# Kernel tuning notes

Measured on AMD Instinct MI355X. Metric: run time of the kernel, lower is better.

Reference implementation:

```python
import jax, jax.numpy as jnp
import numpy as np

NUM_REC = 22
P = 24            # nodes per graph
G = 8192          # graphs in batch
N = G * P         # 196608 nodes
E = N * 4         # 786432 edges (avg degree 4)
F_NODE = 96       # 74 chem features + 22 receptor one-hot
F_EDGE = 16
EPS = 1e-5
NEG_SLOPE = 0.2   # GATv2 default negative_slope


def gatv2(x, src, dst, edge_attr, Wl, bl, Wr, br, We, att, bo):
    """PyG GATv2Conv (heads=1, add_self_loops=True, fill_value='mean'), eval mode."""
    n = x.shape[0]
    # self loops with edge_attr = mean of incoming edge attrs per target node
    deg = jax.ops.segment_sum(jnp.ones_like(dst, dtype=x.dtype), dst, num_segments=n)
    loop_attr = jax.ops.segment_sum(edge_attr, dst, num_segments=n) / jnp.maximum(deg, 1.0)[:, None]
    loop = jnp.arange(n, dtype=src.dtype)
    s = jnp.concatenate([src, loop])           # [E+N] source
    d = jnp.concatenate([dst, loop])           # [E+N] target
    ea = jnp.concatenate([edge_attr, loop_attr], axis=0)
    xl = x @ Wl + bl                           # source transform [n, C]
    xr = x @ Wr + br                           # target transform [n, C]
    m = xl[s] + xr[d] + ea @ We                # [E+N, C]
    e = jax.nn.leaky_relu(m, NEG_SLOPE) @ att  # [E+N] attention logits
    # segment softmax over target nodes (every node has its self loop -> no empty segment)
    emax = jax.ops.segment_max(e, d, num_segments=n)
    ez = jnp.exp(e - emax[d])
    denom = jax.ops.segment_sum(ez, d, num_segments=n)
    alpha = ez / denom[d]
    return jax.ops.segment_sum(alpha[:, None] * xl[s], d, num_segments=n) + bo


def batchnorm(h, gamma, beta):
    # training-style BN (batch statistics, biased var) as in torch BatchNorm1d forward
    mu = h.mean(0)
    var = h.var(0)
    return gamma * (h - mu) * jax.lax.rsqrt(var + EPS) + beta


def setup_inputs() -> dict:
    key = jax.random.key(0)
    ks = jax.random.split(key, 40)
    x = jax.random.normal(ks[0], (N, F_NODE), jnp.float32)
    # intra-graph, self-loop-free edges
    src = jax.random.randint(ks[1], (E,), 0, N)
    off = jax.random.randint(ks[2], (E,), 1, P)
    dst = (src // P) * P + (src % P + off) % P
    edge_index = jnp.stack([src, dst]).astype(jnp.int32)
    edge_attr = jax.random.normal(ks[3], (E, F_EDGE), jnp.float32)
    batch = (jnp.arange(N) // P).astype(jnp.int32)

    def lin(k, i, o):
        return jax.random.normal(k, (i, o), jnp.float32) * 0.1

    def vec(k, o):
        return jax.random.normal(k, (o,), jnp.float32) * 0.1

    Fin = F_NODE - NUM_REC  # 74
    return {
        "x": x, "edge_index": edge_index, "edge_attr": edge_attr, "batch": batch,
        # GATv2 layer 1 (74 -> 32)
        "Wl1": lin(ks[4], Fin, 32), "bl1": vec(ks[5], 32),
        "Wr1": lin(ks[6], Fin, 32), "br1": vec(ks[7], 32),
        "We1": lin(ks[8], F_EDGE, 32), "att1": vec(ks[9], 32), "bo1": vec(ks[10], 32),
        # GATv2 layer 2 (32 -> 8)
        "Wl2": lin(ks[11], 32, 8), "bl2": vec(ks[12], 8),
        "Wr2": lin(ks[13], 32, 8), "br2": vec(ks[14], 8),
        "We2": lin(ks[15], F_EDGE, 8), "att2": vec(ks[16], 8), "bo2": vec(ks[17], 8),
        # BatchNorm affine
        "g1": jnp.ones((32,), jnp.float32), "be1": jnp.zeros((32,), jnp.float32),
        "g2": jnp.ones((8,), jnp.float32), "be2": jnp.zeros((8,), jnp.float32),
        # MLP head (8+22=30 -> 32 -> 16 -> 8 -> 4 -> 2)
        "fc1_W": lin(ks[18], 8 + NUM_REC, 32), "fc1_b": vec(ks[19], 32),
        "fc2_W": lin(ks[20], 32, 16), "fc2_b": vec(ks[21], 16),
        "fc3_W": lin(ks[22], 16, 8), "fc3_b": vec(ks[23], 8),
        "fc4_W": lin(ks[24], 8, 4), "fc4_b": vec(ks[25], 4),
        "out_W": lin(ks[26], 4, 2), "out_b": vec(ks[27], 2),
    }


def reference(x, edge_index, edge_attr, batch,
              Wl1, bl1, Wr1, br1, We1, att1, bo1,
              Wl2, bl2, Wr2, br2, We2, att2, bo2,
              g1, be1, g2, be2,
              fc1_W, fc1_b, fc2_W, fc2_b, fc3_W, fc3_b, fc4_W, fc4_b, out_W, out_b):
    src, dst = edge_index[0], edge_index[1]
    # per-graph receptor features = last NUM_REC cols of the first node of each graph
    first_idx = jnp.searchsorted(batch, jnp.arange(G, dtype=batch.dtype))
    rec_feat = x[first_idx, -NUM_REC:]                       # [G, 22]
    xin = x[:, :-NUM_REC]                                    # [N, 74]

    h = jax.nn.relu(gatv2(xin, src, dst, edge_attr, Wl1, bl1, Wr1, br1, We1, att1, bo1))
    h = batchnorm(h, g1, be1)                                # [N, 32]
    h = jax.nn.sigmoid(gatv2(h, src, dst, edge_attr, Wl2, bl2, Wr2, br2, We2, att2, bo2))
    h = batchnorm(h, g2, be2)                                # [N, 8]

    cnt = jax.ops.segment_sum(jnp.ones((x.shape[0], 1), x.dtype), batch, num_segments=G)
    pooled = jax.ops.segment_sum(h, batch, num_segments=G) / cnt  # global_mean_pool [G, 8]

    z = jnp.concatenate([pooled, rec_feat], axis=1)          # [G, 30]
    z = jax.nn.relu(z @ fc1_W + fc1_b)
    z = jax.nn.relu(z @ fc2_W + fc2_b)
    z = jax.nn.relu(z @ fc3_W + fc3_b)
    z = jax.nn.relu(z @ fc4_W + fc4_b)
    return z @ out_W + out_b                                 # [G, 2]
```

## Files before the change

### kernel.cpp

```cpp
#include <hip/hip_runtime.h>

typedef unsigned short u16;
typedef unsigned int   u32;
typedef __attribute__((ext_vector_type(4))) float f4_t;
typedef __attribute__((ext_vector_type(4))) unsigned short us4_t;

#define GG 8192
#define PP 24
#define NN 196608
#define EE 786432
#define CAP 176

#define oWl1 0
#define oWr1 2368
#define obl1 4736
#define obr1 4768
#define oWe1 4800
#define oatt1 5312
#define obo1 5344
#define oWl2 5376
#define oWr2 5632
#define obl2 5888
#define obr2 5896
#define oWe2 5904
#define oatt2 6032
#define obo2 6040
#define ofc1W 6048
#define ofc1b 7008
#define ofc2W 7040
#define ofc2b 7552
#define ofc3W 7568
#define ofc3b 7696
#define ofc4W 7704
#define ofc4b 7736
#define ooutW 7740
#define ooutb 7748

#define oW1I 0
#define oW2P 4864
#define oB2P 5376

__device__ __forceinline__ float bf2f(u16 u){
  union { u32 i; float f; } x; x.i = ((u32)u) << 16; return x.f;
}
__device__ __forceinline__ u32 fkey(float f){
  int i = __float_as_int(f);
  return (i >= 0) ? (((u32)i) | 0x80000000u) : ~((u32)i);
}
__device__ __forceinline__ float funkey(u32 k){
  u32 i = (k & 0x80000000u) ? (k & 0x7FFFFFFFu) : ~k;
  return __uint_as_float(i);
}
__device__ __forceinline__ float lrelu(float m){ return m > 0.f ? m : 0.2f*m; }
__device__ __forceinline__ float sexp(float a){ return __expf(fminf(a, 0.f)); }
__device__ __forceinline__ float ldf(const void* p, size_t i, int isf){
  return isf ? ((const float*)p)[i] : bf2f(((const u16*)p)[i]);
}

__global__ void k_zero(float* __restrict__ out){
  int i = blockIdx.x*256 + threadIdx.x;
  if(i < GG*2) out[i] = 0.f;
}

__global__ void k_count(const int* __restrict__ dst, int* __restrict__ cnt){
  int e = blockIdx.x*256 + threadIdx.x;
  if(e < EE){
    u32 d = (u32)dst[e];
    if(d < (u32)NN) atomicAdd(&cnt[d], 1);
  }
}

__global__ void k_scanA(const int* __restrict__ cnt, int* __restrict__ offs,
                        int* __restrict__ bsum){
  __shared__ int part[1024];
  int t = threadIdx.x;
  int i = blockIdx.x*1024 + t;
  int c = cnt[i];
  part[t] = c; __syncthreads();
  for(int off=1; off<1024; off<<=1){
    int v = (t>=off) ? part[t-off] : 0;
    __syncthreads();
    part[t] += v;
    __syncthreads();
  }
  offs[i] = part[t] - c;
  if(t==1023) bsum[blockIdx.x] = part[1023];
}

__global__ void k_scanB(int* __restrict__ bsum, int* __restrict__ offs){
  __shared__ int part[256];
  int t = threadIdx.x;
  int c = (t < 192) ? bsum[t] : 0;
  part[t] = c; __syncthreads();
  for(int off=1; off<256; off<<=1){
    int v = (t>=off) ? part[t-off] : 0;
    __syncthreads();
    part[t] += v;
    __syncthreads();
  }
  if(t < 192) bsum[t] = part[t] - c;
  if(t == 255) offs[NN] = part[255];
}

__global__ void k_scanC(int* __restrict__ offs, const int* __restrict__ bsum,
                        int* __restrict__ cursor){
  int t = threadIdx.x;
  int i = blockIdx.x*1024 + t;
  int v = offs[i] + bsum[blockIdx.x];
  offs[i] = v;
  cursor[i] = v;
}

__global__ void k_scatter(const int* __restrict__ src, const int* __restrict__ dst,
                          int* __restrict__ cursor, int* __restrict__ spack){
  int e = blockIdx.x*256 + threadIdx.x;
  if(e < EE){
    u32 d = (u32)dst[e];
    if(d >= (u32)NN) return;
    int g = d / PP;
    int pos = atomicAdd(&cursor[d], 1);
    if((u32)pos < (u32)EE){
      int sl = src[e] - g*PP;
      if((u32)sl > 23u) sl = 0;
      spack[pos] = sl | ((int)(d - g*PP) << 5) | (e << 10);
    }
  }
}

__global__ void k_eaperm(const int* __restrict__ spack, const int* __restrict__ offs,
                         const void* __restrict__ ea, const int* __restrict__ dflag,
                         float* __restrict__ eap){
  int i = blockIdx.x*256 + threadIdx.x;
  if(i >= EE) return;
  if(i >= offs[NN]) return;
  int isf = dflag[0];
  u32 id = ((u32)spack[i]) >> 10;
  if(id >= (u32)EE) id = 0;
  float* o = eap + (size_t)i*16;
  if(isf){
    const float* er = (const float*)ea + (size_t)id*16;
    #pragma unroll
    for(int q=0;q<4;q++) *(f4_t*)(o + q*4) = *(const f4_t*)(er + q*4);
  } else {
    const u16* er = (const u16*)ea + (size_t)id*16;
    #pragma unroll
    for(int c=0;c<16;c++) o[c] = bf2f(er[c]);
  }
}

__global__ void k_eapermP(const int* __restrict__ spack, const int* __restrict__ offs,
                          const void* __restrict__ ea, const int* __restrict__ dflag,
                          const float* __restrict__ wb,
                          float* __restrict__ p1, float* __restrict__ p2){
  int i = blockIdx.x*256 + threadIdx.x;
  if(i >= EE) return;
  if(i >= offs[NN]) return;
  int isf = dflag[0];
  u32 id = ((u32)spack[i]) >> 10;
  if(id >= (u32)EE) id = 0;
  float eav[16];
  if(isf){
    const float* er = (const float*)ea + (size_t)id*16;
    #pragma unroll
    for(int k=0;k<16;k++) eav[k] = er[k];
  } else {
    const u16* er = (const u16*)ea + (size_t)id*16;
    #pragma unroll
    for(int k=0;k<16;k++) eav[k] = bf2f(er[k]);
  }
  float* o1 = p1 + (size_t)i*32;
  #pragma unroll
  for(int c=0;c<32;c+=4){
    float s0=0.f, s1=0.f, s2=0.f, s3=0.f;
    #pragma unroll
    for(int k=0;k<16;k++){
      f4_t w = *(const f4_t*)(wb + oWe1 + k*32 + c);
      s0 += eav[k]*w[0]; s1 += eav[k]*w[1]; s2 += eav[k]*w[2]; s3 += eav[k]*w[3];
    }
    f4_t r; r[0]=s0; r[1]=s1; r[2]=s2; r[3]=s3;
    *(f4_t*)(o1 + c) = r;
  }
  float* o2 = p2 + (size_t)i*8;
  #pragma unroll
  for(int c=0;c<8;c+=4){
    float s0=0.f, s1=0.f, s2=0.f, s3=0.f;
    #pragma unroll
    for(int k=0;k<16;k++){
      f4_t w = *(const f4_t*)(wb + oWe2 + k*8 + c);
      s0 += eav[k]*w[0]; s1 += eav[k]*w[1]; s2 += eav[k]*w[2]; s3 += eav[k]*w[3];
    }
    f4_t r; r[0]=s0; r[1]=s1; r[2]=s2; r[3]=s3;
    *(f4_t*)(o2 + c) = r;
  }
}

__global__ void k_wconv(float* __restrict__ wb, float* __restrict__ wq, int* __restrict__ dflag,
    const u32* __restrict__ xw,
    const void* Wl1, const void* bl1, const void* Wr1, const void* br1,
    const void* We1, const void* att1, const void* bo1,
    const void* Wl2, const void* bl2, const void* Wr2, const void* br2,
    const void* We2, const void* att2, const void* bo2,
    const void* f1W, const void* f1b, const void* f2W, const void* f2b,
    const void* f3W, const void* f3b, const void* f4W, const void* f4b,
    const void* oW,  const void* ob)
{
  __shared__ u32 mx[256];
  int t = threadIdx.x;
  u32 m = 0;
  for(int i=t; i<2048; i+=256){
    u32 e = (xw[i] >> 7) & 0xFFu;
    m = m > e ? m : e;
  }
  mx[t] = m; __syncthreads();
  for(int off=128; off>0; off>>=1){
    if(t<off) mx[t] = mx[t] > mx[t+off] ? mx[t] : mx[t+off];
    __syncthreads();
  }
  int isf = (mx[0] > 140u) ? 1 : 0;
  if(t==0) dflag[0] = isf;
  #define CP(off,src,len) for(int i=t;i<(len);i+=256) wb[(off)+i]=ldf(src,i,isf);
  CP(oWl1,Wl1,2368) CP(oWr1,Wr1,2368) CP(obl1,bl1,32) CP(obr1,br1,32)
  CP(oWe1,We1,512)  CP(oatt1,att1,32) CP(obo1,bo1,32)
  CP(oWl2,Wl2,256)  CP(oWr2,Wr2,256)  CP(obl2,bl2,8)  CP(obr2,br2,8)
  CP(oWe2,We2,128)  CP(oatt2,att2,8)  CP(obo2,bo2,8)
  CP(ofc1W,f1W,960) CP(ofc1b,f1b,32)  CP(ofc2W,f2W,512) CP(ofc2b,f2b,16)
  CP(ofc3W,f3W,128) CP(ofc3b,f3b,8)   CP(ofc4W,f4W,32)  CP(ofc4b,f4b,4)
  CP(ooutW,oW,8)    CP(ooutb,ob,2)
  #undef CP
  for(int i=t; i<76*64; i+=256){
    int k = i>>6, cc = i&63, mat = cc>>5, c = cc&31;
    wq[oW1I + i] = (k < 74) ? ldf(mat ? Wr1 : Wl1, k*32 + c, isf) : 0.f;
  }
}

__global__ void k_prep2(float* __restrict__ wq, const float* __restrict__ wb,
                        const float* __restrict__ stats1){
  int t = threadIdx.x;
  for(int i=t; i<512; i+=256){
    int k = i>>4, cc = i&15, mat = cc>>3, c = cc&7;
    wq[oW2P + i] = stats1[k] * wb[(mat ? oWr2 : oWl2) + k*8 + c];
  }
  if(t < 16){
    int mat = t>>3, c = t&7;
    float s = wb[(mat ? obr2 : obl2) + c];
    for(int k=0;k<32;k++) s += stats1[32+k] * wb[(mat ? oWr2 : oWl2) + k*8 + c];
    wq[oB2P + t] = s;
  }
}

__global__ __launch_bounds__(256, 6) void k_l1stats_p(
    const void* __restrict__ x, const float* __restrict__ p1,
    const float* __restrict__ wb, const float* __restrict__ wq,
    const int* __restrict__ offs, const int* __restrict__ spack, const int* __restrict__ dflag,
    float* __restrict__ p1sum, float* __restrict__ p1sq,
    float* __restrict__ h1)
{
  __shared__ __align__(16) float sXl[24][36];
  __shared__ __align__(16) float sXr[24][36];
  __shared__ __align__(16) float sPS[24][32];
  __shared__ __align__(16) float sPQ[24][32];
  __shared__ float sEv[CAP];
  __shared__ int   sSl[CAP];
  __shared__ int   sRO[25];

  const int t = threadIdx.x;
  const int g = blockIdx.x;
  const int isf = dflag[0];
  const int nb = g*PP;
  const int eb = offs[nb];
  int ecnt = offs[nb+24] - eb;
  if(ecnt < 0) ecnt = 0; if(ecnt > CAP) ecnt = CAP;

  if(t < 25){
    int v = offs[nb+t] - eb;
    if(v < 0) v = 0; if(v > CAP) v = CAP;
    sRO[t] = v;
  }
  for(int i=t; i<ecnt; i+=256){
    int sl = spack[eb+i] & 31; if(sl > 23) sl = 0;
    sSl[i] = sl;
  }

  {
    const int c = t & 31, mat = (t>>5)&1, w = t>>6, cc = t&63;
    const float* gW = wq + oW1I;
    float bi = wb[(mat ? obr1 : obl1) + c];
    float acc[6];
    #pragma unroll
    for(int j=0;j<6;j++) acc[j] = bi;
    if(isf){
      const float* xr0 = (const float*)x + (size_t)(nb + w*6)*96;
      for(int kb=0; kb<19; kb++){
        float w0 = gW[(kb*4+0)*64 + cc];
        float w1 = gW[(kb*4+1)*64 + cc];
        float w2 = gW[(kb*4+2)*64 + cc];
        float w3 = gW[(kb*4+3)*64 + cc];
        #pragma unroll
        for(int j=0;j<6;j++){
          f4_t xv = *(const f4_t*)(xr0 + (size_t)j*96 + kb*4);
          acc[j] += xv[0]*w0 + xv[1]*w1 + xv[2]*w2 + xv[3]*w3;
        }
      }
    } else {
      const u16* xr0 = (const u16*)x + (size_t)(nb + w*6)*96;
      for(int kb=0; kb<19; kb++){
        float w0 = gW[(kb*4+0)*64 + cc];
        float w1 = gW[(kb*4+1)*64 + cc];
        float w2 = gW[(kb*4+2)*64 + cc];
        float w3 = gW[(kb*4+3)*64 + cc];
        #pragma unroll
        for(int j=0;j<6;j++){
          us4_t xv = *(const us4_t*)(xr0 + (size_t)j*96 + kb*4);
          acc[j] += bf2f(xv[0])*w0 + bf2f(xv[1])*w1 + bf2f(xv[2])*w2 + bf2f(xv[3])*w3;
        }
      }
    }
    if(mat){
      #pragma unroll
      for(int j=0;j<6;j++) sXr[w*6+j][c] = acc[j];
    } else {
      #pragma unroll
      for(int j=0;j<6;j++) sXl[w*6+j][c] = acc[j];
    }
  }
  __syncthreads();

  if(t < 192){
    const int r = t >> 3, sub = t & 7;
    const int a = sRO[r], b = sRO[r+1];
    const int deg = b - a;
    const float* att = wb + oatt1;

    float emax = -3.4e38f;
    for(int e=a+sub; e<b; e+=8){
      int sl = sSl[e];
      const float* pe = p1 + (size_t)(eb+e)*32;
      float ev = 0.f;
      #pragma unroll
      for(int q=0;q<8;q++){
        f4_t pv  = *(const f4_t*)(pe + q*4);
        f4_t xlv = *(const f4_t*)&sXl[sl][q*4];
        f4_t xrv = *(const f4_t*)&sXr[r][q*4];
        ev += att[q*4+0]*lrelu(xlv[0]+xrv[0]+pv[0]);
        ev += att[q*4+1]*lrelu(xlv[1]+xrv[1]+pv[1]);
        ev += att[q*4+2]*lrelu(xlv[2]+xrv[2]+pv[2]);
        ev += att[q*4+3]*lrelu(xlv[3]+xrv[3]+pv[3]);
      }
      sEv[e] = ev;
      emax = fmaxf(emax, ev);
    }
    emax = fmaxf(emax, __shfl_xor(emax, 1));
    emax = fmaxf(emax, __shfl_xor(emax, 2));
    emax = fmaxf(emax, __shfl_xor(emax, 4));

    float m0=0.f, m1=0.f, m2=0.f, m3=0.f;
    for(int e=a; e<b; ++e){
      f4_t pv = *(const f4_t*)(p1 + (size_t)(eb+e)*32 + sub*4);
      m0 += pv[0]; m1 += pv[1]; m2 += pv[2]; m3 += pv[3];
    }
    float invd = 1.f / (float)(deg > 0 ? deg : 1);
    float sv;
    {
      int c0 = sub*4;
      sv  = att[c0+0]*lrelu(sXl[r][c0+0] + sXr[r][c0+0] + m0*invd);
      sv += att[c0+1]*lrelu(sXl[r][c0+1] + sXr[r][c0+1] + m1*invd);
      sv += att[c0+2]*lrelu(sXl[r][c0+2] + sXr[r][c0+2] + m2*invd);
      sv += att[c0+3]*lrelu(sXl[r][c0+3] + sXr[r][c0+3] + m3*invd);
    }
    sv += __shfl_xor(sv, 1);
    sv += __shfl_xor(sv, 2);
    sv += __shfl_xor(sv, 4);

    float m = fmaxf(emax, sv);
    float ssum = 0.f;
    for(int e=a+sub; e<b; e+=8){
      float z = sexp(sEv[e] - m);
      sEv[e] = z;
      ssum += z;
    }
    ssum += __shfl_xor(ssum, 1);
    ssum += __shfl_xor(ssum, 2);
    ssum += __shfl_xor(ssum, 4);
    float selfZ = sexp(sv - m);
    float rden = 1.f / fmaxf(ssum + selfZ, 1e-30f);

    float a0=0.f, a1=0.f, a2=0.f, a3=0.f;
    for(int e=a; e<b; ++e){
      float z = sEv[e];
      f4_t xlv = *(const f4_t*)&sXl[sSl[e]][sub*4];
      a0 += z*xlv[0]; a1 += z*xlv[1]; a2 += z*xlv[2]; a3 += z*xlv[3];
    }
    f4_t xself = *(const f4_t*)&sXl[r][sub*4];
    f4_t outv, sqv;
    {
      float o;
      o = (a0 + selfZ*xself[0]) * rden; o = fmaxf(o + wb[obo1+sub*4+0], 0.f); outv[0]=o; sqv[0]=o*o;
      o = (a1 + selfZ*xself[1]) * rden; o = fmaxf(o + wb[obo1+sub*4+1], 0.f); outv[1]=o; sqv[1]=o*o;
      o = (a2 + selfZ*xself[2]) * rden; o = fmaxf(o + wb[obo1+sub*4+2], 0.f); outv[2]=o; sqv[2]=o*o;
      o = (a3 + selfZ*xself[3]) * rden; o = fmaxf(o + wb[obo1+sub*4+3], 0.f); outv[3]=o; sqv[3]=o*o;
    }
    *(f4_t*)&h1[((size_t)nb + r)*32 + sub*4] = outv;
    *(f4_t*)&sPS[r][sub*4] = outv;
    *(f4_t*)&sPQ[r][sub*4] = sqv;
  }
  __syncthreads();
  if(t < 32){
    float s=0.f, q=0.f;
    #pragma unroll
    for(int r=0;r<24;r++){ s += sPS[r][t]; q += sPQ[r][t]; }
    p1sum[g*32+t] = s; p1sq[g*32+t] = q;
  }
}

__global__ __launch_bounds__(256, 6) void k_fused2_p(
    const float* __restrict__ p2,
    const float* __restrict__ wb, const float* __restrict__ wq,
    const float* __restrict__ h1,
    const int* __restrict__ offs, const int* __restrict__ spack,
    float* __restrict__ gsum2, float* __restrict__ gsq2)
{
  __shared__ float sXl2[24][13];
  __shared__ float sXr2[24][13];
  __shared__ float sEv[CAP];
  __shared__ int   sSl[CAP];
  __shared__ int   sRO[25];
  __shared__ float sGS[24][8];
  __shared__ float sGQ[24][8];

  const int t = threadIdx.x;
  const int g = blockIdx.x;
  const int wid = t >> 6;
  const int lane = t & 63;
  const int nb = g*PP;
  const int eb = offs[nb];
  int ecnt = offs[nb+24] - eb;
  if(ecnt < 0) ecnt = 0; if(ecnt > CAP) ecnt = CAP;

  if(t < 25){
    int v = offs[nb+t] - eb;
    if(v < 0) v = 0; if(v > CAP) v = CAP;
    sRO[t] = v;
  }
  for(int i=t; i<ecnt; i+=256){
    int sl = spack[eb+i] & 31; if(sl > 23) sl = 0;
    sSl[i] = sl;
  }
  {
    int rz = wid*6;
    for(int i=lane; i<96; i+=64){
      int rl = i>>4, cc = i&15;
      int r = rz + rl;
      float s = wq[oB2P + cc];
      const float* hr = h1 + ((size_t)nb + r)*32;
      #pragma unroll
      for(int q=0;q<8;q++){
        f4_t hv = *(const f4_t*)(hr + q*4);
        s += hv[0]*wq[oW2P+(q*4+0)*16+cc] + hv[1]*wq[oW2P+(q*4+1)*16+cc]
           + hv[2]*wq[oW2P+(q*4+2)*16+cc] + hv[3]*wq[oW2P+(q*4+3)*16+cc];
      }
      if(cc < 8) sXl2[r][cc] = s; else sXr2[r][cc-8] = s;
    }
  }
  __syncthreads();

  if(t < 192){
    const int r = t >> 3, sub = t & 7;
    const int a = sRO[r], b = sRO[r+1];
    const int deg = b - a;
    const float* att2 = wb + oatt2;

    float emax = -3.4e38f;
    for(int e=a+sub; e<b; e+=8){
      int sl = sSl[e];
      const float* pe = p2 + (size_t)(eb+e)*8;
      float ev = 0.f;
      #pragma unroll
      for(int j=0;j<8;j++)
        ev += att2[j]*lrelu(sXl2[sl][j] + sXr2[r][j] + pe[j]);
      sEv[e] = ev;
      emax = fmaxf(emax, ev);
    }
    emax = fmaxf(emax, __shfl_xor(emax, 1));
    emax = fmaxf(emax, __shfl_xor(emax, 2));
    emax = fmaxf(emax, __shfl_xor(emax, 4));

    float mpc = 0.f;
    for(int e=a; e<b; ++e)
      mpc += p2[(size_t)(eb+e)*8 + sub];
    float invd = 1.f / (float)(deg > 0 ? deg : 1);
    float sv = att2[sub]*lrelu(sXl2[r][sub] + sXr2[r][sub] + mpc*invd);
    sv += __shfl_xor(sv, 1);
    sv += __shfl_xor(sv, 2);
    sv += __shfl_xor(sv, 4);

    float m = fmaxf(emax, sv);
    float ssum = 0.f;
    for(int e=a+sub; e<b; e+=8){
      float z = sexp(sEv[e] - m);
      sEv[e] = z;
      ssum += z;
    }
    ssum += __shfl_xor(ssum, 1);
    ssum += __shfl_xor(ssum, 2);
    ssum += __shfl_xor(ssum, 4);
    float selfZ = sexp(sv - m);
    float rden = 1.f / fmaxf(ssum + selfZ, 1e-30f);

    float acc = 0.f;
    for(int e=a; e<b; ++e)
      acc += sEv[e] * sXl2[sSl[e]][sub];
    float o = (acc + selfZ*sXl2[r][sub]) * rden;
    float s = 1.f / (1.f + __expf(-(o + wb[obo2+sub])));
    sGS[r][sub] = s;
    sGQ[r][sub] = s*s;
  }
  __syncthreads();
  if(t < 8){
    float gs=0.f, gq=0.f;
    #pragma unroll
    for(int r=0;r<24;r++){ gs += sGS[r][t]; gq += sGQ[r][t]; }
    gsum2[g*8+t] = gs; gsq2[g*8+t] = gq;
  }
}

__global__ __launch_bounds__(256, 6) void k_l1stats(
    const void* __restrict__ x, const void* __restrict__ ea, const float* __restrict__ eap,
    const float* __restrict__ wb, const float* __restrict__ wq,
    const int* __restrict__ offs, const int* __restrict__ spack, const int* __restrict__ dflag,
    float* __restrict__ p1sum, float* __restrict__ p1sq,
    float* __restrict__ h1, int use_h1)
{
  __shared__ __align__(16) float sEaF[CAP][16];
  __shared__ __align__(16) float sXl[24][36];
  __shared__ float sXr[24][33];
  __shared__ float sEaSum[24][17];
  __shared__ float sEv[CAP];
  __shared__ int   sSl[CAP];
  __shared__ int   sRO[25];
  __shared__ float sSelfE[24];
  __shared__ float sPS[4][32], sPQ[4][32];

  const int t = threadIdx.x;
  const int g = blockIdx.x;
  const int wid = t >> 6;
  const int lane = t & 63;
  const int isf = dflag[0];
  const int nb = g*PP;
  const int eb = offs[nb];
  int ecnt = offs[nb+24] - eb; if(ecnt < 0) ecnt = 0; if(ecnt > CAP) ecnt = CAP;

  if(t < 25){
    int v = offs[nb+t] - eb;
    if(v < 0) v = 0; if(v > CAP) v = CAP;
    sRO[t] = v;
  }
  if(eap){
    for(int i=t; i<ecnt; i+=256) sSl[i] = spack[eb+i] & 1023;
    for(int i=t; i<ecnt*4; i+=256){
      int e = i>>2, q = i&3;
      *(f4_t*)&sEaF[e][q*4] = *(const f4_t*)(eap + ((size_t)(eb+e))*16 + q*4);
    }
  } else {
    for(int i=t; i<ecnt; i+=256){
      int sp = spack[eb+i];
      sSl[i] = sp & 1023;
      u32 id = ((u32)sp) >> 10;
      if(id >= (u32)EE) id = 0;
      if(isf){
        const float* er = (const float*)ea + (size_t)id*16;
        #pragma unroll
        for(int q=0;q<4;q++) *(f4_t*)&sEaF[i][q*4] = *(const f4_t*)(er + q*4);
      } else {
        #pragma unroll
        for(int c=0;c<16;c++) sEaF[i][c] = bf2f(((const u16*)ea)[(size_t)id*16 + c]);
      }
    }
  }
  {
    int rz = wid*6;
    for(int i=lane; i<6*17; i+=64) sEaSum[rz + i/17][i%17] = 0.f;
  }

  {
    const int c = t & 31, mat = (t>>5)&1, w = wid, cc = t&63;
    const float* gW = wq + oW1I;
    float bi = wb[(mat ? obr1 : obl1) + c];
    float acc[6];
    #pragma unroll
    for(int j=0;j<6;j++) acc[j] = bi;
    if(isf){
      const float* xr0 = (const float*)x + (size_t)(nb + w*6)*96;
      for(int kb=0; kb<19; kb++){
        float w0 = gW[(kb*4+0)*64 + cc];
        float w1 = gW[(kb*4+1)*64 + cc];
        float w2 = gW[(kb*4+2)*64 + cc];
        float w3 = gW[(kb*4+3)*64 + cc];
        #pragma unroll
        for(int j=0;j<6;j++){
          f4_t xv = *(const f4_t*)(xr0 + (size_t)j*96 + kb*4);
          acc[j] += xv[0]*w0 + xv[1]*w1 + xv[2]*w2 + xv[3]*w3;
        }
      }
    } else {
      const u16* xr0 = (const u16*)x + (size_t)(nb + w*6)*96;
      for(int kb=0; kb<19; kb++){
        float w0 = gW[(kb*4+0)*64 + cc];
        float w1 = gW[(kb*4+1)*64 + cc];
        float w2 = gW[(kb*4+2)*64 + cc];
        float w3 = gW[(kb*4+3)*64 + cc];
        #pragma unroll
        for(int j=0;j<6;j++){
          us4_t xv = *(const us4_t*)(xr0 + (size_t)j*96 + kb*4);
          acc[j] += bf2f(xv[0])*w0 + bf2f(xv[1])*w1 + bf2f(xv[2])*w2 + bf2f(xv[3])*w3;
        }
      }
    }
    if(mat){
      #pragma unroll
      for(int j=0;j<6;j++) sXr[w*6+j][c] = acc[j];
    } else {
      #pragma unroll
      for(int j=0;j<6;j++) sXl[w*6+j][c] = acc[j];
    }
  }
  __syncthreads();

  const int r0 = wid*6;
  const int a0 = sRO[r0], a1 = sRO[r0+6];
  const int c = t & 31, eo = (t>>5)&1;

  float wr[16];
  #pragma unroll
  for(int k=0;k<16;k++) wr[k] = wb[oWe1 + k*32 + c];
  const float av = wb[oatt1 + c];
  const float bv = wb[obo1 + c];

  for(int base=a0; base<a1; base+=2){
    int e = base + eo;
    bool valid = (e < a1);
    int ec = valid ? e : a0;
    int sp = sSl[ec];
    int sl = sp & 31; if(sl > 23) sl = 0;
    int dl = (sp >> 5) & 31; if(dl > 23) dl = 0;
    f4_t A0 = *(const f4_t*)&sEaF[ec][0];
    f4_t A1 = *(const f4_t*)&sEaF[ec][4];
    f4_t A2 = *(const f4_t*)&sEaF[ec][8];
    f4_t A3 = *(const f4_t*)&sEaF[ec][12];
    float p = A0[0]*wr[0]+A0[1]*wr[1]+A0[2]*wr[2]+A0[3]*wr[3]
            + A1[0]*wr[4]+A1[1]*wr[5]+A1[2]*wr[6]+A1[3]*wr[7]
            + A2[0]*wr[8]+A2[1]*wr[9]+A2[2]*wr[10]+A2[3]*wr[11]
            + A3[0]*wr[12]+A3[1]*wr[13]+A3[2]*wr[14]+A3[3]*wr[15];
    if(valid && c < 16) atomicAdd(&sEaSum[dl][c], sEaF[ec][c]);
    float v = lrelu(sXl[sl][c] + sXr[dl][c] + p) * av;
    v += __shfl_xor(v, 16);
    v += __shfl_xor(v, 8);
    v += __shfl_xor(v, 4);
    v += __shfl_xor(v, 2);
    v += __shfl_xor(v, 1);
    if(valid && c == 0) sEv[e] = v;
  }

  #pragma unroll
  for(int rp=0; rp<3; rp++){
    int r = r0 + rp*2 + eo;
    int deg = sRO[r+1] - sRO[r];
    float invd = 1.f / (float)(deg > 0 ? deg : 1);
    float mp = 0.f;
    #pragma unroll
    for(int k=0;k<16;k++) mp += sEaSum[r][k] * wr[k];
    float v = lrelu(sXl[r][c] + sXr[r][c] + mp*invd) * av;
    v += __shfl_xor(v, 16);
    v += __shfl_xor(v, 8);
    v += __shfl_xor(v, 4);
    v += __shfl_xor(v, 2);
    v += __shfl_xor(v, 1);
    if(c == 0) sSelfE[r] = v;
  }

  float ps = 0.f, pq = 0.f;
  const int h = (t >> 5) & 1;
  #pragma unroll
  for(int j=0;j<6;j++){
    int r = r0 + j;
    int a = sRO[r], b = sRO[r+1];
    float selfE = sSelfE[r];
    float mx = -3.4e38f;
    for(int e=a+lane; e<b; e+=64) mx = fmaxf(mx, sEv[e]);
    mx = fmaxf(mx, __shfl_xor(mx, 32));
    mx = fmaxf(mx, __shfl_xor(mx, 16));
    mx = fmaxf(mx, __shfl_xor(mx, 8));
    mx = fmaxf(mx, __shfl_xor(mx, 4));
    mx = fmaxf(mx, __shfl_xor(mx, 2));
    mx = fmaxf(mx, __shfl_xor(mx, 1));
    float m = fmaxf(mx, selfE);
    float ds = 0.f;
    for(int e=a+lane; e<b; e+=64){
      float z = sexp(sEv[e] - m);
      sEv[e] = z;
      ds += z;
    }
    ds += __shfl_xor(ds, 32);
    ds += __shfl_xor(ds, 16);
    ds += __shfl_xor(ds, 8);
    ds += __shfl_xor(ds, 4);
    ds += __shfl_xor(ds, 2);
    ds += __shfl_xor(ds, 1);
    float selfZ = sexp(selfE - m);
    float rden = 1.f / fmaxf(ds + selfZ, 1e-30f);
    float acc = 0.f;
    for(int e=a+h; e<b; e+=2){
      int sl = sSl[e] & 31; if(sl > 23) sl = 0;
      acc += sEv[e] * sXl[sl][c];
    }
    acc += __shfl_xor(acc, 32);
    float out = (acc + selfZ * sXl[r][c]) * rden;
    out = fmaxf(out + bv, 0.f);
    if(h == 0){
      if(use_h1) h1[((size_t)nb + r)*32 + c] = out;
      ps += out; pq += out*out;
    }
  }
  if(h == 0){ sPS[wid][c] = ps; sPQ[wid][c] = pq; }
  __syncthreads();
  if(t < 32){
    p1sum[g*32+t] = sPS[0][t]+sPS[1][t]+sPS[2][t]+sPS[3][t];
    p1sq[g*32+t]  = sPQ[0][t]+sPQ[1][t]+sPQ[2][t]+sPQ[3][t];
  }
}

__global__ void k_reduce(const float* __restrict__ ps, const float* __restrict__ pq,
                         const void* __restrict__ gamma, const void* __restrict__ beta,
                         const int* __restrict__ dflag,
                         float* __restrict__ stats, int F){
  __shared__ float rs[256], rq[256];
  int f = blockIdx.x, t = threadIdx.x;
  float s=0.f, q=0.f;
  for(int g=t; g<GG; g+=256){ s += ps[g*F+f]; q += pq[g*F+f]; }
  rs[t]=s; rq[t]=q; __syncthreads();
  for(int off=128; off>0; off>>=1){
    if(t<off){ rs[t]+=rs[t+off]; rq[t]+=rq[t+off]; }
    __syncthreads();
  }
  if(t==0){
    int isf = dflag[0];
    float mu  = rs[0] * (1.f/(float)NN);
    float var = rq[0] * (1.f/(float)NN) - mu*mu;
    if(var < 0.f) var = 0.f;
    float sc  = ldf(gamma,f,isf) / sqrtf(var + 1e-5f);
    stats[f]   = sc;
    stats[F+f] = ldf(beta,f,isf) - mu*sc;
  }
}

__global__ __launch_bounds__(256, 6) void k_fused2_h1(
    const void* __restrict__ ea, const float* __restrict__ eap,
    const float* __restrict__ wb, const float* __restrict__ wq,
    const float* __restrict__ h1,
    const int* __restrict__ offs, const int* __restrict__ spack, const int* __restrict__ dflag,
    float* __restrict__ gsum2, float* __restrict__ gsq2)
{
  __shared__ __align__(16) float sEaF[CAP][16];
  __shared__ float sXl2[24][12], sXr2[24][12];
  __shared__ float sEaSum[24][17];
  __shared__ float sEv[CAP];
  __shared__ int   sSl[CAP];
  __shared__ int   sRO[25];
  __shared__ float sSelfE[24];
  __shared__ float sGS[4][8], sGQ[4][8];

  const int t = threadIdx.x;
  const int g = blockIdx.x;
  const int wid = t >> 6;
  const int lane = t & 63;
  const int isf = dflag[0];
  const int nb = g*PP;
  const int eb = offs[nb];
  int ecnt = offs[nb+24] - eb; if(ecnt < 0) ecnt = 0; if(ecnt > CAP) ecnt = CAP;

  if(t < 25){
    int v = offs[nb+t] - eb;
    if(v < 0) v = 0; if(v > CAP) v = CAP;
    sRO[t] = v;
  }
  if(eap){
    for(int i=t; i<ecnt; i+=256) sSl[i] = spack[eb+i] & 1023;
    for(int i=t; i<ecnt*4; i+=256){
      int e = i>>2, q = i&3;
      *(f4_t*)&sEaF[e][q*4] = *(const f4_t*)(eap + ((size_t)(eb+e))*16 + q*4);
    }
  } else {
    for(int i=t; i<ecnt; i+=256){
      int sp = spack[eb+i];
      sSl[i] = sp & 1023;
      u32 id = ((u32)sp) >> 10;
      if(id >= (u32)EE) id = 0;
      if(isf){
        const float* er = (const float*)ea + (size_t)id*16;
        #pragma unroll
        for(int q=0;q<4;q++) *(f4_t*)&sEaF[i][q*4] = *(const f4_t*)(er + q*4);
      } else {
        #pragma unroll
        for(int c=0;c<16;c++) sEaF[i][c] = bf2f(((const u16*)ea)[(size_t)id*16 + c]);
      }
    }
  }
  {
    int rz = wid*6;
    for(int i=lane; i<6*17; i+=64) sEaSum[rz + i/17][i%17] = 0.f;
    for(int i=lane; i<96; i+=64){
      int rl = i>>4, cc = i&15;
      int r = rz + rl;
      float s = wq[oB2P + cc];
      const float* hr = h1 + ((size_t)nb + r)*32;
      #pragma unroll
      for(int q=0;q<8;q++){
        f4_t hv = *(const f4_t*)(hr + q*4);
        s += hv[0]*wq[oW2P+(q*4+0)*16+cc] + hv[1]*wq[oW2P+(q*4+1)*16+cc]
           + hv[2]*wq[oW2P+(q*4+2)*16+cc] + hv[3]*wq[oW2P+(q*4+3)*16+cc];
      }
      if(cc < 8) sXl2[r][cc] = s; else sXr2[r][cc-8] = s;
    }
  }
  __syncthreads();

  const int r0 = wid*6;
  const int a0 = sRO[r0], a1 = sRO[r0+6];
  const int c = t & 7;
  const int eo = lane >> 3;

  float wr[16];
  #pragma unroll
  for(int k=0;k<16;k++) wr[k] = wb[oWe2 + k*8 + c];
  const float av = wb[oatt2 + c];
  const float bv = wb[obo2 + c];

  for(int base=a0; base<a1; base+=8){
    int e = base + eo;
    bool valid = (e < a1);
    int ec = valid ? e : a0;
    int sp = sSl[ec];
    int sl = sp & 31; if(sl > 23) sl = 0;
    int dl = (sp >> 5) & 31; if(dl > 23) dl = 0;
    f4_t A0 = *(const f4_t*)&sEaF[ec][0];
    f4_t A1 = *(const f4_t*)&sEaF[ec][4];
    f4_t A2 = *(const f4_t*)&sEaF[ec][8];
    f4_t A3 = *(const f4_t*)&sEaF[ec][12];
    float p = A0[0]*wr[0]+A0[1]*wr[1]+A0[2]*wr[2]+A0[3]*wr[3]
            + A1[0]*wr[4]+A1[1]*wr[5]+A1[2]*wr[6]+A1[3]*wr[7]
            + A2[0]*wr[8]+A2[1]*wr[9]+A2[2]*wr[10]+A2[3]*wr[11]
            + A3[0]*wr[12]+A3[1]*wr[13]+A3[2]*wr[14]+A3[3]*wr[15];
    if(valid){
      atomicAdd(&sEaSum[dl][c],   sEaF[ec][c]);
      atomicAdd(&sEaSum[dl][c+8], sEaF[ec][c+8]);
    }
    float v = lrelu(sXl2[sl][c] + sXr2[dl][c] + p) * av;
    v += __shfl_xor(v, 4);
    v += __shfl_xor(v, 2);
    v += __shfl_xor(v, 1);
    if(valid && c == 0) sEv[e] = v;
  }

  {
    int rr = r0 + (eo < 6 ? eo : 0);
    bool valid = (eo < 6);
    int deg = sRO[rr+1] - sRO[rr];
    float invd = 1.f / (float)(deg > 0 ? deg : 1);
    float mp = 0.f;
    #pragma unroll
    for(int k=0;k<16;k++) mp += sEaSum[rr][k] * wr[k];
    float v = lrelu(sXl2[rr][c] + sXr2[rr][c] + mp*invd) * av;
    v += __shfl_xor(v, 4);
    v += __shfl_xor(v, 2);
    v += __shfl_xor(v, 1);
    if(valid && c == 0) sSelfE[rr] = v;
  }

  float gs = 0.f, gq = 0.f;
  #pragma unroll
  for(int j=0;j<6;j++){
    int r = r0 + j;
    int a = sRO[r], b = sRO[r+1];
    float selfE = sSelfE[r];
    float mx = -3.4e38f;
    for(int e=a+lane; e<b; e+=64) mx = fmaxf(mx, sEv[e]);
    mx = fmaxf(mx, __shfl_xor(mx, 32));
    mx = fmaxf(mx, __shfl_xor(mx, 16));
    mx = fmaxf(mx, __shfl_xor(mx, 8));
    mx = fmaxf(mx, __shfl_xor(mx, 4));
    mx = fmaxf(mx, __shfl_xor(mx, 2));
    mx = fmaxf(mx, __shfl_xor(mx, 1));
    float m = fmaxf(mx, selfE);
    float ds = 0.f;
    for(int e=a+lane; e<b; e+=64){
      float z = sexp(sEv[e] - m);
      sEv[e] = z;
      ds += z;
    }
    ds += __shfl_xor(ds, 32);
    ds += __shfl_xor(ds, 16);
    ds += __shfl_xor(ds, 8);
    ds += __shfl_xor(ds, 4);
    ds += __shfl_xor(ds, 2);
    ds += __shfl_xor(ds, 1);
    float selfZ = sexp(selfE - m);
    float rden = 1.f / fmaxf(ds + selfZ, 1e-30f);
    float acc = 0.f;
    for(int e=a+eo; e<b; e+=8){
      int sl = sSl[e] & 31; if(sl > 23) sl = 0;
      acc += sEv[e] * sXl2[sl][c];
    }
    acc += __shfl_xor(acc, 8);
    acc += __shfl_xor(acc, 16);
    acc += __shfl_xor(acc, 32);
    float out = (acc + selfZ * sXl2[r][c]) * rden;
    float s = 1.f / (1.f + __expf(-(out + bv)));
    if(eo == 0){ gs += s; gq += s*s; }
  }
  if(eo == 0){ sGS[wid][c] = gs; sGQ[wid][c] = gq; }
  __syncthreads();
  if(t < 8){
    gsum2[g*8+t] = sGS[0][t]+sGS[1][t]+sGS[2][t]+sGS[3][t];
    gsq2[g*8+t]  = sGQ[0][t]+sGQ[1][t]+sGQ[2][t]+sGQ[3][t];
  }
}

__global__ __launch_bounds__(256) void k_fused2_rec(
    const void* __restrict__ x, const void* __restrict__ ea,
    const float* __restrict__ wb, const float* __restrict__ stats1,
    const int* __restrict__ offs, const int* __restrict__ spack, const int* __restrict__ dflag,
    float* __restrict__ gsum2, float* __restrict__ gsq2)
{
  __shared__ float sXrow[24][76];
  __shared__ float sEaF[CAP][17];
  __shared__ __align__(16) float sXl[24][36];
  __shared__ __align__(16) float sXr[24][36];
  __shared__ __align__(16) float sOut[24][36];
  __shared__ float sH[24][33];
  __shared__ float sXl2[24][12], sXr2[24][12], sOut2[24][12];
  __shared__ float sEapSum[24][32];
  __shared__ float sEv[CAP], sEz[CAP];
  __shared__ int   sSp[CAP];
  __shared__ int   sDeg[24];
  __shared__ u32   sMaxU[24];
  __shared__ float sMaxF[24], sDen[24], sSelfZ[24];
  __shared__ float sAtt[32], sBo[32], sSc[32], sSh[32];

  const int t = threadIdx.x;
  const int g = blockIdx.x;
  const int isf = dflag[0];
  int eb = offs[g*24], ee = offs[(g+1)*24];
  if(eb < 0) eb = 0; if(eb > EE) eb = EE;
  if(ee < eb) ee = eb; if(ee > EE) ee = EE;
  int ecnt = ee - eb; if(ecnt > CAP) ecnt = CAP;

  for(int i=t; i<24*74; i+=256){
    int r = i/74, c = i%74;
    sXrow[r][c] = ldf(x, (size_t)(g*PP + r)*96 + c, isf);
  }
  for(int i=t; i<CAP; i+=256) sSp[i] = (i<ecnt) ? spack[eb+i] : 0;
  if(t < 32){ sAtt[t]=wb[oatt1+t]; sBo[t]=wb[obo1+t]; sSc[t]=stats1[t]; sSh[t]=stats1[32+t]; }
  if(t < 24){ sDeg[t]=0; sMaxU[t]=0u; sDen[t]=0.f; }
  for(int i=t; i<24*32; i+=256) sEapSum[i>>5][i&31] = 0.f;
  __syncthreads();
  for(int i=t; i<CAP*16; i+=256){
    int e = i>>4, c = i&15;
    float v = 0.f;
    if(e < ecnt){
      u32 id = ((u32)sSp[e]) >> 10;
      if(id >= (u32)EE) id = 0;
      v = ldf(ea, (size_t)id*16 + c, isf);
    }
    sEaF[e][c] = v;
  }
  __syncthreads();

  {
    int c = t & 31, rr0 = t >> 5;
    for(int r = rr0; r < 24; r += 8){
      float al = wb[obl1+c], ar = wb[obr1+c];
      for(int k=0;k<74;k++){
        float xv = sXrow[r][k];
        al += xv * wb[oWl1 + k*32 + c];
        ar += xv * wb[oWr1 + k*32 + c];
      }
      sXl[r][c] = al; sXr[r][c] = ar;
    }
  }
  __syncthreads();

  for(int e=t; e<ecnt; e+=256){
    int sp = sSp[e];
    int sl = sp & 31; if(sl > 23) sl = 0;
    int dl = (sp >> 5) & 31; if(dl > 23) dl = 0;
    float ev = 0.f;
    for(int c=0;c<32;c++){
      float p = 0.f;
      for(int k=0;k<16;k++) p += sEaF[e][k] * wb[oWe1 + k*32 + c];
      atomicAdd(&sEapSum[dl][c], p);
      ev += lrelu(sXl[sl][c] + sXr[dl][c] + p) * sAtt[c];
    }
    sEv[e] = ev;
    atomicMax(&sMaxU[dl], fkey(ev));
    atomicAdd(&sDeg[dl], 1);
  }
  __syncthreads();

  if(t < 24){
    float invd = 1.f / (float)(sDeg[t] > 0 ? sDeg[t] : 1);
    float ev = 0.f;
    for(int c=0;c<32;c++)
      ev += lrelu(sXl[t][c] + sXr[t][c] + sEapSum[t][c]*invd) * sAtt[c];
    float mxv = (sDeg[t] > 0) ? fmaxf(funkey(sMaxU[t]), ev) : ev;
    sMaxF[t] = mxv;
    float z = sexp(ev - mxv);
    sSelfZ[t] = z;
    sDen[t] = z;
  }
  __syncthreads();

  for(int e=t; e<ecnt; e+=256){
    int dl = (sSp[e]>>5)&31; if(dl > 23) dl = 0;
    float z = sexp(sEv[e] - sMaxF[dl]);
    sEz[e] = z;
    atomicAdd(&sDen[dl], z);
  }
  __syncthreads();

  for(int e=t; e<ecnt; e+=256){
    int dl = (sSp[e]>>5)&31; if(dl > 23) dl = 0;
    sEz[e] /= fmaxf(sDen[dl], 1e-30f);
  }
  if(t < 24) sSelfZ[t] /= fmaxf(sDen[t], 1e-30f);
  __syncthreads();

  for(int o=t; o<24*8; o+=256){
    int nl = o >> 3, cq = (o & 7)*4;
    float al = sSelfZ[nl];
    f4_t xv = *(const f4_t*)&sXl[nl][cq];
    f4_t r;
    #pragma unroll
    for(int j=0;j<4;j++) r[j] = al*xv[j];
    *(f4_t*)&sOut[nl][cq] = r;
  }
  __syncthreads();

  for(int o=t; o<ecnt*8; o+=256){
    int e = o >> 3, cq = (o & 7)*4;
    int sp = sSp[e];
    int sl = sp & 31; if(sl > 23) sl = 0;
    int dl = (sp >> 5) & 31; if(dl > 23) dl = 0;
    float al = sEz[e];
    f4_t xv = *(const f4_t*)&sXl[sl][cq];
    atomicAdd(&sOut[dl][cq+0], al*xv[0]);
    atomicAdd(&sOut[dl][cq+1], al*xv[1]);
    atomicAdd(&sOut[dl][cq+2], al*xv[2]);
    atomicAdd(&sOut[dl][cq+3], al*xv[3]);
  }
  __syncthreads();

  for(int i=t; i<24*32; i+=256){
    int r = i>>5, c = i&31;
    float v = fmaxf(sOut[r][c] + sBo[c], 0.f);
    sH[r][c] = v*sSc[c] + sSh[c];
  }
  __syncthreads();
  if(t < 24){ sDeg[t]=0; sMaxU[t]=0u; sDen[t]=0.f; }
  for(int i=t; i<24*8; i+=256) sEapSum[i>>3][i&7] = 0.f;
  __syncthreads();

  if(t < 24*8*2){
    int mat = t/192, rem = t%192, r = rem/8, c = rem&7;
    const float* Wm = wb + (mat ? oWr2 : oWl2);
    float s = wb[(mat ? obr2 : obl2) + c];
    for(int k=0;k<32;k++) s += sH[r][k]*Wm[k*8+c];
    if(mat) sXr2[r][c] = s; else sXl2[r][c] = s;
  }
  __syncthreads();

  for(int e=t; e<ecnt; e+=256){
    int sp = sSp[e];
    int sl = sp & 31; if(sl > 23) sl = 0;
    int dl = (sp >> 5) & 31; if(dl > 23) dl = 0;
    float ev = 0.f;
    for(int c=0;c<8;c++){
      float p = 0.f;
      for(int k=0;k<16;k++) p += sEaF[e][k] * wb[oWe2 + k*8 + c];
      atomicAdd(&sEapSum[dl][c], p);
      ev += lrelu(sXl2[sl][c] + sXr2[dl][c] + p) * wb[oatt2+c];
    }
    sEv[e] = ev;
    atomicMax(&sMaxU[dl], fkey(ev));
    atomicAdd(&sDeg[dl], 1);
  }
  __syncthreads();

  if(t < 24){
    float invd = 1.f / (float)(sDeg[t] > 0 ? sDeg[t] : 1);
    float ev = 0.f;
    for(int c=0;c<8;c++)
      ev += lrelu(sXl2[t][c] + sXr2[t][c] + sEapSum[t][c]*invd) * wb[oatt2+c];
    float mxv = (sDeg[t] > 0) ? fmaxf(funkey(sMaxU[t]), ev) : ev;
    sMaxF[t] = mxv;
    float z = sexp(ev - mxv);
    sSelfZ[t] = z;
    sDen[t] = z;
  }
  __syncthreads();

  for(int e=t; e<ecnt; e+=256){
    int dl = (sSp[e]>>5)&31; if(dl > 23) dl = 0;
    float z = sexp(sEv[e] - sMaxF[dl]);
    sEz[e] = z;
    atomicAdd(&sDen[dl], z);
  }
  __syncthreads();

  for(int e=t; e<ecnt; e+=256){
    int dl = (sSp[e]>>5)&31; if(dl > 23) dl = 0;
    sEz[e] /= fmaxf(sDen[dl], 1e-30f);
  }
  if(t < 24) sSelfZ[t] /= fmaxf(sDen[t], 1e-30f);
  __syncthreads();

  for(int o=t; o<24*8; o+=256){
    int nl = o >> 3, c = o & 7;
    sOut2[nl][c] = sSelfZ[nl] * sXl2[nl][c];
  }
  __syncthreads();

  for(int o=t; o<ecnt*8; o+=256){
    int e = o >> 3, c = o & 7;
    int sp = sSp[e];
    int sl = sp & 31; if(sl > 23) sl = 0;
    int dl = (sp >> 5) & 31; if(dl > 23) dl = 0;
    atomicAdd(&sOut2[dl][c], sEz[e]*sXl2[sl][c]);
  }
  __syncthreads();

  if(t < 8){
    float gs=0.f, gq=0.f;
    for(int nl=0; nl<24; nl++){
      float v = sOut2[nl][t] + wb[obo2+t];
      float s = 1.f / (1.f + __expf(-v));
      gs += s; gq += s*s;
    }
    gsum2[g*8+t] = gs; gsq2[g*8+t] = gq;
  }
}

__global__ __launch_bounds__(256) void k_mlp(
    const float* __restrict__ gsum2, const float* __restrict__ stats2,
    const void* __restrict__ x, const int* __restrict__ dflag,
    const float* __restrict__ wb, float* __restrict__ out)
{
  __shared__ float w[1702];
  int t = threadIdx.x;
  for(int i=t; i<1702; i+=256) w[i] = wb[6048+i];
  __syncthreads();
  int g = blockIdx.x*256 + t;
  int isf = dflag[0];
  float a[30], b[32];
  for(int c=0;c<8;c++) a[c] = stats2[c]*(gsum2[(size_t)g*8+c]*(1.f/24.f)) + stats2[8+c];
  size_t xoff = (size_t)g*PP*96 + 74;
  for(int j=0;j<22;j++) a[8+j] = ldf(x, xoff+j, isf);
  for(int o=0;o<32;o++){ float s = w[960+o];  for(int i=0;i<30;i++) s += a[i]*w[i*32+o];      b[o]=fmaxf(s,0.f); }
  for(int o=0;o<16;o++){ float s = w[1504+o]; for(int i=0;i<32;i++) s += b[i]*w[992+i*16+o];  a[o]=fmaxf(s,0.f); }
  for(int o=0;o<8;o++){  float s = w[1648+o]; for(int i=0;i<16;i++) s += a[i]*w[1520+i*8+o];  b[o]=fmaxf(s,0.f); }
  for(int o=0;o<4;o++){  float s = w[1688+o]; for(int i=0;i<8;i++)  s += b[i]*w[1656+i*4+o];  a[o]=fmaxf(s,0.f); }
  for(int o=0;o<2;o++){
    float s = w[1700+o];
    for(int i=0;i<4;i++) s += a[i]*w[1692+i*2+o];
    out[(size_t)g*2+o] = s;
  }
}

extern "C" void kernel_launch(void* const* d_in, const int* in_sizes, int n_in,
                              void* d_out, int out_size, void* d_ws, size_t ws_size,
                              hipStream_t stream)
{
  (void)in_sizes; (void)n_in; (void)out_size;
  const void* x    = d_in[0];
  const int* eidx  = (const int*)d_in[1];
  const void* ea   = d_in[2];

  const int* srcA = eidx;
  const int* dstA = eidx + EE;

  constexpr size_t O_WB    = 0;
  constexpr size_t O_WQ    = 32768;
  constexpr size_t O_OFFS  = 57344;
  constexpr size_t O_CUR   = O_OFFS + (size_t)(NN+512)*4;
  constexpr size_t O_SPACK = O_CUR  + (size_t)NN*4;
  constexpr size_t O_P1S   = O_SPACK + (size_t)EE*4;
  constexpr size_t O_P1Q   = O_P1S   + (size_t)GG*32*4;
  constexpr size_t O_ST1   = O_P1Q   + (size_t)GG*32*4;
  constexpr size_t O_GS2   = O_ST1   + 256;
  constexpr size_t O_GQ2   = O_GS2   + (size_t)GG*8*4;
  constexpr size_t O_ST2   = O_GQ2   + (size_t)GG*8*4;
  constexpr size_t O_FLAG  = O_ST2   + 256;
  constexpr size_t REQUIRED_BASE = O_FLAG + 256;
  constexpr size_t O_H1    = REQUIRED_BASE;
  constexpr size_t REQUIRED_BIG = O_H1 + (size_t)NN*32*4;
  constexpr size_t O_EAP1  = REQUIRED_BIG;
  constexpr size_t O_EAP2  = O_EAP1 + (size_t)EE*32*4;
  constexpr size_t REQUIRED_P = O_EAP2 + (size_t)EE*8*4;
  constexpr size_t REQUIRED_EAP16 = O_EAP1 + (size_t)EE*16*4;

  if(ws_size < REQUIRED_BASE){
    k_zero<<<(GG*2+255)/256, 256, 0, stream>>>((float*)d_out);
    return;
  }
  const int use_h1  = (ws_size >= REQUIRED_BIG)   ? 1 : 0;
  const int use_p   = (ws_size >= REQUIRED_P)     ? 1 : 0;
  const int use_eap = (!use_p && ws_size >= REQUIRED_EAP16) ? 1 : 0;

  char* W = (char*)d_ws;
  float* wb     = (float*)(W + O_WB);
  float* wq     = (float*)(W + O_WQ);
  int*   offs   = (int*)(W + O_OFFS);
  int*   bsum   = offs + NN + 64;
  int*   cnt    = (int*)(W + O_CUR);
  int*   cursor = (int*)(W + O_CUR);
  int*   spack  = (int*)(W + O_SPACK);
  float* p1sum  = (float*)(W + O_P1S);
  float* p1sq   = (float*)(W + O_P1Q);
  float* stats1 = (float*)(W + O_ST1);
  float* gsum2  = (float*)(W + O_GS2);
  float* gsq2   = (float*)(W + O_GQ2);
  float* stats2 = (float*)(W + O_ST2);
  int*   dflag  = (int*)(W + O_FLAG);
  float* h1     = (float*)(W + O_H1);
  float* eap1   = (float*)(W + O_EAP1);
  float* eap2   = (float*)(W + O_EAP2);

  hipMemsetAsync(cnt, 0, (size_t)NN*sizeof(int), stream);
  k_count  <<<EE/256, 256, 0, stream>>>(dstA, cnt);
  k_scanA  <<<192, 1024, 0, stream>>>(cnt, offs, bsum);
  k_scanB  <<<1, 256, 0, stream>>>(bsum, offs);
  k_scanC  <<<192, 1024, 0, stream>>>(offs, bsum, cursor);
  k_scatter<<<EE/256, 256, 0, stream>>>(srcA, dstA, cursor, spack);
  k_wconv  <<<1, 256, 0, stream>>>(wb, wq, dflag, (const u32*)x,
            d_in[4], d_in[5], d_in[6], d_in[7], d_in[8], d_in[9], d_in[10],
            d_in[11], d_in[12], d_in[13], d_in[14], d_in[15], d_in[16], d_in[17],
            d_in[22], d_in[23], d_in[24], d_in[25], d_in[26], d_in[27],
            d_in[28], d_in[29], d_in[30], d_in[31]);
  if(use_p){
    k_eapermP<<<EE/256, 256, 0, stream>>>(spack, offs, ea, dflag, wb, eap1, eap2);
    k_l1stats_p<<<GG, 256, 0, stream>>>(x, eap1, wb, wq, offs, spack, dflag,
                                        p1sum, p1sq, h1);
  } else {
    if(use_eap)
      k_eaperm<<<EE/256, 256, 0, stream>>>(spack, offs, ea, dflag, eap1);
    k_l1stats<<<GG, 256, 0, stream>>>(x, ea, use_eap ? eap1 : (float*)nullptr,
                                      wb, wq, offs, spack, dflag,
                                      p1sum, p1sq, h1, use_h1);
  }
  k_reduce <<<32, 256, 0, stream>>>(p1sum, p1sq, d_in[18], d_in[19], dflag, stats1, 32);
  k_prep2  <<<1, 256, 0, stream>>>(wq, wb, stats1);
  if(use_p)
    k_fused2_p<<<GG, 256, 0, stream>>>(eap2, wb, wq, h1, offs, spack, gsum2, gsq2);
  else if(use_h1)
    k_fused2_h1<<<GG, 256, 0, stream>>>(ea, use_eap ? eap1 : (float*)nullptr,
                                        wb, wq, h1, offs, spack, dflag, gsum2, gsq2);
  else
    k_fused2_rec<<<GG, 256, 0, stream>>>(x, ea, wb, stats1, offs, spack, dflag, gsum2, gsq2);
  k_reduce <<<8, 256, 0, stream>>>(gsum2, gsq2, d_in[20], d_in[21], dflag, stats2, 8);
  k_mlp    <<<GG/256, 256, 0, stream>>>(gsum2, stats2, x, dflag, wb, (float*)d_out);
}
```

Measured before the change: 686.4 us.

## Compute layer-1 edge projection in-block from permuted edge attrs into LDS

The permutation kernel no longer writes the 32-wide layer-1 edge projection (ea@We1) to global memory. It writes only the raw 16-float permuted edge attributes plus the 8-wide layer-2 projection. The layer-1 stats kernel now recomputes the 32-wide projection per graph into a shared-memory tile and reads it from LDS in the softmax and mean loops. This halves the global traffic for that intermediate at the cost of extra per-block FLOPs and about 25KB more LDS, and the occupancy hint is lowered from 6 to 4 blocks.

```diff
diff --git a/kernel.cpp b/kernel.cpp
--- a/kernel.cpp
+++ b/kernel.cpp
@@ -148,10 +148,10 @@
   }
 }
 
-__global__ void k_eapermP(const int* __restrict__ spack, const int* __restrict__ offs,
+__global__ void k_eapermB(const int* __restrict__ spack, const int* __restrict__ offs,
                           const void* __restrict__ ea, const int* __restrict__ dflag,
                           const float* __restrict__ wb,
-                          float* __restrict__ p1, float* __restrict__ p2){
+                          float* __restrict__ eap, float* __restrict__ p2){
   int i = blockIdx.x*256 + threadIdx.x;
   if(i >= EE) return;
   if(i >= offs[NN]) return;
@@ -168,17 +168,11 @@
     #pragma unroll
     for(int k=0;k<16;k++) eav[k] = bf2f(er[k]);
   }
-  float* o1 = p1 + (size_t)i*32;
+  float* o = eap + (size_t)i*16;
   #pragma unroll
-  for(int c=0;c<32;c+=4){
-    float s0=0.f, s1=0.f, s2=0.f, s3=0.f;
-    #pragma unroll
-    for(int k=0;k<16;k++){
-      f4_t w = *(const f4_t*)(wb + oWe1 + k*32 + c);
-      s0 += eav[k]*w[0]; s1 += eav[k]*w[1]; s2 += eav[k]*w[2]; s3 += eav[k]*w[3];
-    }
-    f4_t r; r[0]=s0; r[1]=s1; r[2]=s2; r[3]=s3;
-    *(f4_t*)(o1 + c) = r;
+  for(int q=0;q<4;q++){
+    f4_t r; r[0]=eav[q*4+0]; r[1]=eav[q*4+1]; r[2]=eav[q*4+2]; r[3]=eav[q*4+3];
+    *(f4_t*)(o + q*4) = r;
   }
   float* o2 = p2 + (size_t)i*8;
   #pragma unroll
@@ -248,13 +242,14 @@
   }
 }
 
-__global__ __launch_bounds__(256, 6) void k_l1stats_p(
-    const void* __restrict__ x, const float* __restrict__ p1,
+__global__ __launch_bounds__(256, 4) void k_l1stats_p(
+    const void* __restrict__ x, const float* __restrict__ eap,
     const float* __restrict__ wb, const float* __restrict__ wq,
     const int* __restrict__ offs, const int* __restrict__ spack, const int* __restrict__ dflag,
     float* __restrict__ p1sum, float* __restrict__ p1sq,
     float* __restrict__ h1)
 {
+  __shared__ __align__(16) float sP[CAP][36];
   __shared__ __align__(16) float sXl[24][36];
   __shared__ __align__(16) float sXr[24][36];
   __shared__ __align__(16) float sPS[24][32];
@@ -323,6 +318,20 @@
       for(int j=0;j<6;j++) sXl[w*6+j][c] = acc[j];
     }
   }
+
+  for(int i=t; i<ecnt*8; i+=256){
+    int e = i>>3, q = i&7;
+    const float* er = eap + (size_t)(eb+e)*16;
+    float s0=0.f, s1=0.f, s2=0.f, s3=0.f;
+    #pragma unroll
+    for(int k=0;k<16;k++){
+      float ev = er[k];
+      f4_t w = *(const f4_t*)(wb + oWe1 + k*32 + q*4);
+      s0 += ev*w[0]; s1 += ev*w[1]; s2 += ev*w[2]; s3 += ev*w[3];
+    }
+    f4_t r; r[0]=s0; r[1]=s1; r[2]=s2; r[3]=s3;
+    *(f4_t*)&sP[e][q*4] = r;
+  }
   __syncthreads();
 
   if(t < 192){
@@ -334,11 +343,10 @@
     float emax = -3.4e38f;
     for(int e=a+sub; e<b; e+=8){
       int sl = sSl[e];
-      const float* pe = p1 + (size_t)(eb+e)*32;
       float ev = 0.f;
       #pragma unroll
       for(int q=0;q<8;q++){
-        f4_t pv  = *(const f4_t*)(pe + q*4);
+        f4_t pv  = *(const f4_t*)&sP[e][q*4];
         f4_t xlv = *(const f4_t*)&sXl[sl][q*4];
         f4_t xrv = *(const f4_t*)&sXr[r][q*4];
         ev += att[q*4+0]*lrelu(xlv[0]+xrv[0]+pv[0]);
@@ -355,7 +363,7 @@
 
     float m0=0.f, m1=0.f, m2=0.f, m3=0.f;
     for(int e=a; e<b; ++e){
-      f4_t pv = *(const f4_t*)(p1 + (size_t)(eb+e)*32 + sub*4);
+      f4_t pv = *(const f4_t*)&sP[e][sub*4];
       m0 += pv[0]; m1 += pv[1]; m2 += pv[2]; m3 += pv[3];
     }
     float invd = 1.f / (float)(deg > 0 ? deg : 1);
@@ -1202,8 +1210,8 @@
   constexpr size_t O_H1    = REQUIRED_BASE;
   constexpr size_t REQUIRED_BIG = O_H1 + (size_t)NN*32*4;
   constexpr size_t O_EAP1  = REQUIRED_BIG;
-  constexpr size_t O_EAP2  = O_EAP1 + (size_t)EE*32*4;
-  constexpr size_t REQUIRED_P = O_EAP2 + (size_t)EE*8*4;
+  constexpr size_t O_P2    = O_EAP1 + (size_t)EE*16*4;
+  constexpr size_t REQUIRED_P = O_P2 + (size_t)EE*8*4;
   constexpr size_t REQUIRED_EAP16 = O_EAP1 + (size_t)EE*16*4;
 
   if(ws_size < REQUIRED_BASE){
@@ -1231,7 +1239,7 @@
   int*   dflag  = (int*)(W + O_FLAG);
   float* h1     = (float*)(W + O_H1);
   float* eap1   = (float*)(W + O_EAP1);
-  float* eap2   = (float*)(W + O_EAP2);
+  float* p2     = (float*)(W + O_P2);
 
   hipMemsetAsync(cnt, 0, (size_t)NN*sizeof(int), stream);
   k_count  <<<EE/256, 256, 0, stream>>>(dstA, cnt);
@@ -1245,7 +1253,7 @@
             d_in[22], d_in[23], d_in[24], d_in[25], d_in[26], d_in[27],
             d_in[28], d_in[29], d_in[30], d_in[31]);
   if(use_p){
-    k_eapermP<<<EE/256, 256, 0, stream>>>(spack, offs, ea, dflag, wb, eap1, eap2);
+    k_eapermB<<<EE/256, 256, 0, stream>>>(spack, offs, ea, dflag, wb, eap1, p2);
     k_l1stats_p<<<GG, 256, 0, stream>>>(x, eap1, wb, wq, offs, spack, dflag,
                                         p1sum, p1sq, h1);
   } else {
@@ -1258,7 +1266,7 @@
   k_reduce <<<32, 256, 0, stream>>>(p1sum, p1sq, d_in[18], d_in[19], dflag, stats1, 32);
   k_prep2  <<<1, 256, 0, stream>>>(wq, wb, stats1);
   if(use_p)
-    k_fused2_p<<<GG, 256, 0, stream>>>(eap2, wb, wq, h1, offs, spack, gsum2, gsq2);
+    k_fused2_p<<<GG, 256, 0, stream>>>(p2, wb, wq, h1, offs, spack, gsum2, gsq2);
   else if(use_h1)
     k_fused2_h1<<<GG, 256, 0, stream>>>(ea, use_eap ? eap1 : (float*)nullptr,
                                         wb, wq, h1, offs, spack, dflag, gsum2, gsq2);
```

Measured after the change: 591.1 us. -13.9%, faster.
